# Kernel optimization log

Hardware: AMD Instinct MI355X
Metric: run time of the kernel (lower is better)

## Reference

```python
import jax, jax.numpy as jnp
import numpy as np

B, N, D = 8192, 50, 64


def setup_inputs() -> dict:
    key = jax.random.key(0)
    k1, k2, k3 = jax.random.split(key, 3)
    F = jax.random.normal(k1, (B, N, D), dtype=jnp.float32)
    # xavier_normal for square DxD linear: std = sqrt(2/(D+D)) = 1/sqrt(D)
    std = 1.0 / np.sqrt(D)
    K_w = jax.random.normal(k2, (D, D), dtype=jnp.float32) * std
    Q_w = jax.random.normal(k3, (D, D), dtype=jnp.float32) * std
    return {"F": F, "K_w": K_w, "Q_w": Q_w}


def reference(F, K_w, Q_w):
    # K(F): Linear with weight K_w (torch convention: x @ W^T)
    KF = jnp.einsum('bnd,ed->bne', F, K_w)          # [B,N,D]
    # S = F @ K(F)^T
    S = jnp.einsum('bnd,bmd->bnm', F, KF)           # [B,N,N]
    # out[b,n,d] = sum_m S[b,n,m] * F[b,n,d] * F[b,m,d]
    #            = F[b,n,d] * (S @ F)[b,n,d]   (algebraic fusion of the
    #              bnd,bmd->bnmd outer product + weighted sum over m)
    out = F * jnp.einsum('bnm,bmd->bnd', S, F)      # [B,N,D]
    # residual branch: Q(F)
    out = out + jnp.einsum('bnd,ed->bne', F, Q_w)
    return out
```

## Files before the change

kernel.cpp:

```cpp
#include <hip/hip_runtime.h>

typedef __attribute__((ext_vector_type(8))) short s16x8;
typedef __attribute__((ext_vector_type(4))) short s16x4;
typedef __attribute__((ext_vector_type(4))) float f32x4;

#define ST 72

__device__ __forceinline__ short f2bf(float f) {
    unsigned u = __builtin_bit_cast(unsigned, f);
    u += 0x7FFFu + ((u >> 16) & 1u);
    return (short)(u >> 16);
}

__global__ __launch_bounds__(256, 3) void sam3e_fused(
    const float* __restrict__ F, const float* __restrict__ Kw,
    const float* __restrict__ Qw, float* __restrict__ out)
{
    __shared__ __align__(16) short sKw[64 * ST];
    __shared__ __align__(16) short sQw[64 * ST];
    __shared__ __align__(16) short sA [64 * ST];
    __shared__ __align__(16) short sAT[64 * ST];
    __shared__ __align__(16) short sKS[64 * ST];

    const int b    = blockIdx.x;
    const int tid  = threadIdx.x;
    const int wave = tid >> 6;
    const int lane = tid & 63;
    const int col  = lane & 15;
    const int quad = lane >> 4;

    const f32x4* Kv = (const f32x4*)Kw;
    const f32x4* Qv = (const f32x4*)Qw;
    #pragma unroll
    for (int i = tid; i < 1024; i += 256) {
        int e = i >> 4, d4 = (i & 15) << 2;
        f32x4 kv = Kv[i], qv = Qv[i];
        s16x4 hk = { f2bf(kv.x), f2bf(kv.y), f2bf(kv.z), f2bf(kv.w) };
        s16x4 hq = { f2bf(qv.x), f2bf(qv.y), f2bf(qv.z), f2bf(qv.w) };
        *(s16x4*)&sKw[e * ST + d4] = hk;
        *(s16x4*)&sQw[e * ST + d4] = hq;
    }

    const f32x4* Fv = (const f32x4*)(F + (size_t)b * 3200);
    const f32x4 zero4 = {0.f, 0.f, 0.f, 0.f};
    #pragma unroll
    for (int i = tid; i < 1024; i += 256) {
        int n = i >> 4, d4 = (i & 15) << 2;
        f32x4 v = (n < 50) ? Fv[i] : zero4;
        s16x4 h = { f2bf(v.x), f2bf(v.y), f2bf(v.z), f2bf(v.w) };
        *(s16x4*)&sA[n * ST + d4] = h;
        sAT[(d4 + 0) * ST + n] = h.x;
        sAT[(d4 + 1) * ST + n] = h.y;
        sAT[(d4 + 2) * ST + n] = h.z;
        sAT[(d4 + 3) * ST + n] = h.w;
    }
    __syncthreads();

    const int mt   = wave;
    const int arow = (mt * 16 + col) * ST;

    s16x8 a0 = *(const s16x8*)&sA[arow + quad * 8];
    s16x8 a1 = *(const s16x8*)&sA[arow + 32 + quad * 8];

    #pragma unroll
    for (int nt = 0; nt < 4; ++nt) {
        const int brow = (nt * 16 + col) * ST;
        s16x8 b0 = *(const s16x8*)&sKw[brow + quad * 8];
        s16x8 b1 = *(const s16x8*)&sKw[brow + 32 + quad * 8];
        f32x4 acc = {0.f, 0.f, 0.f, 0.f};
        acc = __builtin_amdgcn_mfma_f32_16x16x32_bf16(a0, b0, acc, 0, 0, 0);
        acc = __builtin_amdgcn_mfma_f32_16x16x32_bf16(a1, b1, acc, 0, 0, 0);
        #pragma unroll
        for (int r = 0; r < 4; ++r)
            sKS[(mt * 16 + quad * 4 + r) * ST + nt * 16 + col] = f2bf(acc[r]);
    }
    __syncthreads();

    f32x4 Sacc[4];
    #pragma unroll
    for (int nt = 0; nt < 4; ++nt) {
        const int brow = (nt * 16 + col) * ST;
        s16x8 b0 = *(const s16x8*)&sKS[brow + quad * 8];
        s16x8 b1 = *(const s16x8*)&sKS[brow + 32 + quad * 8];
        f32x4 acc = {0.f, 0.f, 0.f, 0.f};
        acc = __builtin_amdgcn_mfma_f32_16x16x32_bf16(a0, b0, acc, 0, 0, 0);
        acc = __builtin_amdgcn_mfma_f32_16x16x32_bf16(a1, b1, acc, 0, 0, 0);
        Sacc[nt] = acc;
    }
    __syncthreads();
    #pragma unroll
    for (int nt = 0; nt < 4; ++nt)
        #pragma unroll
        for (int r = 0; r < 4; ++r)
            sKS[(mt * 16 + quad * 4 + r) * ST + nt * 16 + col] = f2bf(Sacc[nt][r]);
    __syncthreads();

    s16x8 sa0 = *(const s16x8*)&sKS[arow + quad * 8];
    s16x8 sa1 = *(const s16x8*)&sKS[arow + 32 + quad * 8];
    const float* Fb = F   + (size_t)b * 3200;
    float*       Ob = out + (size_t)b * 3200;
    #pragma unroll
    for (int nt = 0; nt < 4; ++nt) {
        const int brow = (nt * 16 + col) * ST;
        s16x8 bt0 = *(const s16x8*)&sAT[brow + quad * 8];
        s16x8 bt1 = *(const s16x8*)&sAT[brow + 32 + quad * 8];
        s16x8 bq0 = *(const s16x8*)&sQw[brow + quad * 8];
        s16x8 bq1 = *(const s16x8*)&sQw[brow + 32 + quad * 8];
        f32x4 t = {0.f, 0.f, 0.f, 0.f};
        f32x4 q = {0.f, 0.f, 0.f, 0.f};
        t = __builtin_amdgcn_mfma_f32_16x16x32_bf16(sa0, bt0, t, 0, 0, 0);
        t = __builtin_amdgcn_mfma_f32_16x16x32_bf16(sa1, bt1, t, 0, 0, 0);
        q = __builtin_amdgcn_mfma_f32_16x16x32_bf16(a0,  bq0, q, 0, 0, 0);
        q = __builtin_amdgcn_mfma_f32_16x16x32_bf16(a1,  bq1, q, 0, 0, 0);
        #pragma unroll
        for (int r = 0; r < 4; ++r) {
            int n = mt * 16 + quad * 4 + r;
            if (n < 50) {
                int idx = n * 64 + nt * 16 + col;
                Ob[idx] = Fb[idx] * t[r] + q[r];
            }
        }
    }
}

extern "C" void kernel_launch(void* const* d_in, const int* in_sizes, int n_in,
                              void* d_out, int out_size, void* d_ws, size_t ws_size,
                              hipStream_t stream) {
    const float* F  = (const float*)d_in[0];
    const float* Kw = (const float*)d_in[1];
    const float* Qw = (const float*)d_in[2];
    float* out = (float*)d_out;
    sam3e_fused<<<8192, 256, 0, stream>>>(F, Kw, Qw, out);
}
```

Baseline: 253.3 us.

## Make blocks persistent over 8 batches with register prefetch of next F tile

Each block now processes 8 batch elements in a loop, so the K and Q weights are loaded and converted to bf16 once per block rather than once per batch. The F tile for the next batch is prefetched into registers during the current batch's compute. The A operand fragments are read straight from global memory instead of from a shared sA array, which is removed, and occupancy is raised to 4 blocks per CU. The trade-off is only 1024 blocks, which lowers parallelism, and loop-carried barriers.

```diff
diff --git a/kernel.cpp b/kernel.cpp
--- a/kernel.cpp
+++ b/kernel.cpp
@@ -5,119 +5,144 @@
 typedef __attribute__((ext_vector_type(4))) float f32x4;
 
 #define ST 72
+#define NB 8
+#define MFMA __builtin_amdgcn_mfma_f32_16x16x32_bf16
 
 __device__ __forceinline__ short f2bf(float f) {
     unsigned u = __builtin_bit_cast(unsigned, f);
     u += 0x7FFFu + ((u >> 16) & 1u);
     return (short)(u >> 16);
 }
+__device__ __forceinline__ s16x8 cvt8(f32x4 a, f32x4 b) {
+    s16x8 r = { f2bf(a.x), f2bf(a.y), f2bf(a.z), f2bf(a.w),
+                f2bf(b.x), f2bf(b.y), f2bf(b.z), f2bf(b.w) };
+    return r;
+}
 
-__global__ __launch_bounds__(256, 3) void sam3e_fused(
+__global__ __launch_bounds__(256, 4) void sam3e_v2(
     const float* __restrict__ F, const float* __restrict__ Kw,
     const float* __restrict__ Qw, float* __restrict__ out)
 {
     __shared__ __align__(16) short sKw[64 * ST];
     __shared__ __align__(16) short sQw[64 * ST];
-    __shared__ __align__(16) short sA [64 * ST];
     __shared__ __align__(16) short sAT[64 * ST];
     __shared__ __align__(16) short sKS[64 * ST];
 
-    const int b    = blockIdx.x;
     const int tid  = threadIdx.x;
-    const int wave = tid >> 6;
+    const int w    = tid >> 6;
     const int lane = tid & 63;
     const int col  = lane & 15;
-    const int quad = lane >> 4;
+    const int q    = lane >> 4;
 
-    const f32x4* Kv = (const f32x4*)Kw;
-    const f32x4* Qv = (const f32x4*)Qw;
-    #pragma unroll
-    for (int i = tid; i < 1024; i += 256) {
-        int e = i >> 4, d4 = (i & 15) << 2;
-        f32x4 kv = Kv[i], qv = Qv[i];
-        s16x4 hk = { f2bf(kv.x), f2bf(kv.y), f2bf(kv.z), f2bf(kv.w) };
-        s16x4 hq = { f2bf(qv.x), f2bf(qv.y), f2bf(qv.z), f2bf(qv.w) };
-        *(s16x4*)&sKw[e * ST + d4] = hk;
-        *(s16x4*)&sQw[e * ST + d4] = hq;
+    {
+        const int e  = tid & 63;
+        const int dg = tid >> 6;
+        const f32x4* Kv = (const f32x4*)(Kw + e * 64 + dg * 16);
+        const f32x4* Qv = (const f32x4*)(Qw + e * 64 + dg * 16);
+        #pragma unroll
+        for (int k = 0; k < 4; ++k) {
+            f32x4 kv = Kv[k], qv = Qv[k];
+            s16x4 hk = { f2bf(kv.x), f2bf(kv.y), f2bf(kv.z), f2bf(kv.w) };
+            s16x4 hq = { f2bf(qv.x), f2bf(qv.y), f2bf(qv.z), f2bf(qv.w) };
+            *(s16x4*)&sKw[e * ST + dg * 16 + k * 4] = hk;
+            *(s16x4*)&sQw[e * ST + dg * 16 + k * 4] = hq;
+        }
     }
 
-    const f32x4* Fv = (const f32x4*)(F + (size_t)b * 3200);
-    const f32x4 zero4 = {0.f, 0.f, 0.f, 0.f};
-    #pragma unroll
-    for (int i = tid; i < 1024; i += 256) {
-        int n = i >> 4, d4 = (i & 15) << 2;
-        f32x4 v = (n < 50) ? Fv[i] : zero4;
-        s16x4 h = { f2bf(v.x), f2bf(v.y), f2bf(v.z), f2bf(v.w) };
-        *(s16x4*)&sA[n * ST + d4] = h;
-        sAT[(d4 + 0) * ST + n] = h.x;
-        sAT[(d4 + 1) * ST + n] = h.y;
-        sAT[(d4 + 2) * ST + n] = h.z;
-        sAT[(d4 + 3) * ST + n] = h.w;
+    const int sn  = tid & 63;
+    const int sdg = tid >> 6;
+    const f32x4 z4 = {0.f, 0.f, 0.f, 0.f};
+
+    int b = blockIdx.x * NB;
+    f32x4 pf0 = z4, pf1 = z4, pf2 = z4, pf3 = z4;
+    if (sn < 50) {
+        const f32x4* Fr = (const f32x4*)(F + (size_t)b * 3200 + sn * 64 + sdg * 16);
+        pf0 = Fr[0]; pf1 = Fr[1]; pf2 = Fr[2]; pf3 = Fr[3];
     }
-    __syncthreads();
 
-    const int mt   = wave;
-    const int arow = (mt * 16 + col) * ST;
+    for (int it = 0; it < NB; ++it, ++b) {
+        const float* Fb = F   + (size_t)b * 3200;
+        float*       Ob = out + (size_t)b * 3200;
 
-    s16x8 a0 = *(const s16x8*)&sA[arow + quad * 8];
-    s16x8 a1 = *(const s16x8*)&sA[arow + 32 + quad * 8];
+        __syncthreads();
 
-    #pragma unroll
-    for (int nt = 0; nt < 4; ++nt) {
-        const int brow = (nt * 16 + col) * ST;
-        s16x8 b0 = *(const s16x8*)&sKw[brow + quad * 8];
-        s16x8 b1 = *(const s16x8*)&sKw[brow + 32 + quad * 8];
-        f32x4 acc = {0.f, 0.f, 0.f, 0.f};
-        acc = __builtin_amdgcn_mfma_f32_16x16x32_bf16(a0, b0, acc, 0, 0, 0);
-        acc = __builtin_amdgcn_mfma_f32_16x16x32_bf16(a1, b1, acc, 0, 0, 0);
+        {
+            const int d0 = sdg * 16;
+            short h[16] = { f2bf(pf0.x), f2bf(pf0.y), f2bf(pf0.z), f2bf(pf0.w),
+                            f2bf(pf1.x), f2bf(pf1.y), f2bf(pf1.z), f2bf(pf1.w),
+                            f2bf(pf2.x), f2bf(pf2.y), f2bf(pf2.z), f2bf(pf2.w),
+                            f2bf(pf3.x), f2bf(pf3.y), f2bf(pf3.z), f2bf(pf3.w) };
+            #pragma unroll
+            for (int i = 0; i < 16; ++i) sAT[(d0 + i) * ST + sn] = h[i];
+        }
+
+        s16x8 a0, a1;
+        {
+            const int row = 16 * w + col;
+            f32x4 v0 = z4, v1 = z4, v2 = z4, v3 = z4;
+            if (row < 50) {
+                const f32x4* Fr = (const f32x4*)(Fb + row * 64);
+                v0 = Fr[2 * q]; v1 = Fr[2 * q + 1];
+                v2 = Fr[8 + 2 * q]; v3 = Fr[8 + 2 * q + 1];
+            }
+            a0 = cvt8(v0, v1); a1 = cvt8(v2, v3);
+        }
+
         #pragma unroll
-        for (int r = 0; r < 4; ++r)
-            sKS[(mt * 16 + quad * 4 + r) * ST + nt * 16 + col] = f2bf(acc[r]);
-    }
-    __syncthreads();
+        for (int nt = 0; nt < 4; ++nt) {
+            const short* yb = &sKw[(16 * nt + col) * ST + 8 * q];
+            f32x4 acc = {0.f, 0.f, 0.f, 0.f};
+            acc = MFMA(a0, *(const s16x8*)yb,        acc, 0, 0, 0);
+            acc = MFMA(a1, *(const s16x8*)(yb + 32), acc, 0, 0, 0);
+            #pragma unroll
+            for (int r = 0; r < 4; ++r)
+                sKS[(16 * w + 4 * q + r) * ST + 16 * nt + col] = f2bf(acc[r]);
+        }
+        __syncthreads();
 
-    f32x4 Sacc[4];
-    #pragma unroll
-    for (int nt = 0; nt < 4; ++nt) {
-        const int brow = (nt * 16 + col) * ST;
-        s16x8 b0 = *(const s16x8*)&sKS[brow + quad * 8];
-        s16x8 b1 = *(const s16x8*)&sKS[brow + 32 + quad * 8];
-        f32x4 acc = {0.f, 0.f, 0.f, 0.f};
-        acc = __builtin_amdgcn_mfma_f32_16x16x32_bf16(a0, b0, acc, 0, 0, 0);
-        acc = __builtin_amdgcn_mfma_f32_16x16x32_bf16(a1, b1, acc, 0, 0, 0);
-        Sacc[nt] = acc;
-    }
-    __syncthreads();
-    #pragma unroll
-    for (int nt = 0; nt < 4; ++nt)
+        f32x4 S[4];
         #pragma unroll
-        for (int r = 0; r < 4; ++r)
-            sKS[(mt * 16 + quad * 4 + r) * ST + nt * 16 + col] = f2bf(Sacc[nt][r]);
-    __syncthreads();
+        for (int nt = 0; nt < 4; ++nt) {
+            const short* yb = &sKS[(16 * nt + col) * ST + 8 * q];
+            f32x4 acc = {0.f, 0.f, 0.f, 0.f};
+            acc = MFMA(a0, *(const s16x8*)yb,        acc, 0, 0, 0);
+            acc = MFMA(a1, *(const s16x8*)(yb + 32), acc, 0, 0, 0);
+            S[nt] = acc;
+        }
 
-    s16x8 sa0 = *(const s16x8*)&sKS[arow + quad * 8];
-    s16x8 sa1 = *(const s16x8*)&sKS[arow + 32 + quad * 8];
-    const float* Fb = F   + (size_t)b * 3200;
-    float*       Ob = out + (size_t)b * 3200;
-    #pragma unroll
-    for (int nt = 0; nt < 4; ++nt) {
-        const int brow = (nt * 16 + col) * ST;
-        s16x8 bt0 = *(const s16x8*)&sAT[brow + quad * 8];
-        s16x8 bt1 = *(const s16x8*)&sAT[brow + 32 + quad * 8];
-        s16x8 bq0 = *(const s16x8*)&sQw[brow + quad * 8];
-        s16x8 bq1 = *(const s16x8*)&sQw[brow + 32 + quad * 8];
-        f32x4 t = {0.f, 0.f, 0.f, 0.f};
-        f32x4 q = {0.f, 0.f, 0.f, 0.f};
-        t = __builtin_amdgcn_mfma_f32_16x16x32_bf16(sa0, bt0, t, 0, 0, 0);
-        t = __builtin_amdgcn_mfma_f32_16x16x32_bf16(sa1, bt1, t, 0, 0, 0);
-        q = __builtin_amdgcn_mfma_f32_16x16x32_bf16(a0,  bq0, q, 0, 0, 0);
-        q = __builtin_amdgcn_mfma_f32_16x16x32_bf16(a1,  bq1, q, 0, 0, 0);
+        if (it + 1 < NB && sn < 50) {
+            const f32x4* Fr = (const f32x4*)(Fb + 3200 + sn * 64 + sdg * 16);
+            pf0 = Fr[0]; pf1 = Fr[1]; pf2 = Fr[2]; pf3 = Fr[3];
+        }
+
+        __syncthreads();
         #pragma unroll
-        for (int r = 0; r < 4; ++r) {
-            int n = mt * 16 + quad * 4 + r;
-            if (n < 50) {
-                int idx = n * 64 + nt * 16 + col;
-                Ob[idx] = Fb[idx] * t[r] + q[r];
+        for (int nt = 0; nt < 4; ++nt)
+            #pragma unroll
+            for (int r = 0; r < 4; ++r)
+                sKS[(16 * w + 4 * q + r) * ST + 16 * nt + col] = f2bf(S[nt][r]);
+        __syncthreads();
+
+        const short* sb = &sKS[(16 * w + col) * ST + 8 * q];
+        s16x8 s0 = *(const s16x8*)sb;
+        s16x8 s1 = *(const s16x8*)(sb + 32);
+        #pragma unroll
+        for (int nt = 0; nt < 4; ++nt) {
+            const short* tb = &sAT[(16 * nt + col) * ST + 8 * q];
+            const short* qb = &sQw[(16 * nt + col) * ST + 8 * q];
+            f32x4 t  = {0.f, 0.f, 0.f, 0.f};
+            f32x4 qa = {0.f, 0.f, 0.f, 0.f};
+            t  = MFMA(s0, *(const s16x8*)tb,        t,  0, 0, 0);
+            t  = MFMA(s1, *(const s16x8*)(tb + 32), t,  0, 0, 0);
+            qa = MFMA(a0, *(const s16x8*)qb,        qa, 0, 0, 0);
+            qa = MFMA(a1, *(const s16x8*)(qb + 32), qa, 0, 0, 0);
+            #pragma unroll
+            for (int r = 0; r < 4; ++r) {
+                const int n = 16 * w + 4 * q + r;
+                if (n < 50) {
+                    const int idx = n * 64 + 16 * nt + col;
+                    Ob[idx] = Fb[idx] * t[r] + qa[r];
+                }
             }
         }
     }
@@ -130,5 +155,5 @@
     const float* Kw = (const float*)d_in[1];
     const float* Qw = (const float*)d_in[2];
     float* out = (float*)d_out;
-    sam3e_fused<<<8192, 256, 0, stream>>>(F, Kw, Qw, out);
+    sam3e_v2<<<8192 / NB, 256, 0, stream>>>(F, Kw, Qw, out);
 }
```

New measurement: 221.5 us. 12.6% less time.
